# Optimization experiments

Hardware: AMD Instinct MI355X
Metric: run time of the kernel (lower is better)

The kernel has to match this reference:

```python
import jax, jax.numpy as jnp
import numpy as np

SIG_DEPTH = 4  # matches sig_depth init arg


def _outer(a, b):
    # flattened tensor product: [B, m] x [B, n] -> [B, m*n] (row-major, matches signatory layout)
    return (a[:, :, None] * b[:, None, :]).reshape(a.shape[0], -1)


def setup_inputs() -> dict:
    key = jax.random.key(0)
    k1, k2 = jax.random.split(key)
    B, L, Cin = 64, 256, 7
    out_dim = 512
    C = Cin + 1
    sig_channels = sum(C ** k for k in range(1, SIG_DEPTH + 1))  # 4680
    inp = jax.random.normal(k1, (B, L, Cin), dtype=jnp.float32)
    W = jax.random.normal(k2, (out_dim, sig_channels), dtype=jnp.float32) * 0.02
    b = jnp.zeros((out_dim,), dtype=jnp.float32)
    return {"inp": inp, "W": W, "b": b}


def reference(inp, W, b):
    B, L, Cin = inp.shape
    # Augment: prepend time channel linspace(0, 1, L), keep original channels
    t = jnp.broadcast_to(jnp.linspace(0.0, 1.0, L, dtype=inp.dtype)[None, :, None], (B, L, 1))
    x = jnp.concatenate([t, inp], axis=-1)  # [B, L, C]
    C = Cin + 1
    d = SIG_DEPTH
    dx = jnp.transpose(x[:, 1:] - x[:, :-1], (1, 0, 2))  # [L-1, B, C] increments
    init = tuple(jnp.zeros((B, C ** (k + 1)), x.dtype) for k in range(d))  # identity signature (all zero levels)

    def step(levels, v):
        # exp(v) in the truncated tensor algebra: e_k = v^{(x)k} / k!
        e = [v]
        for k in range(1, d):
            e.append(_outer(e[-1], v) / (k + 1))
        # Chen's identity: new_k = a_k + e_k + sum_{i=1}^{k-1} a_i (x) e_{k-i}
        new = []
        for k in range(d):
            acc = levels[k] + e[k]
            for i in range(k):
                acc = acc + _outer(levels[i], e[k - 1 - i])
            new.append(acc)
        sig = jnp.concatenate(new, axis=-1)  # [B, sig_channels]
        return tuple(new), sig

    _, sigs = jax.lax.scan(step, init, dx)  # [L-1, B, sig_channels] (stream=True)
    sigs = jnp.transpose(sigs, (1, 0, 2))   # [B, L-1, sig_channels]
    return sigs @ W.T + b                   # [B, L-1, out_dim]
```

## Files before the change

kernel.cpp:

```cpp
#include <hip/hip_runtime.h>
#include <hip/hip_bf16.h>

#define BATCH 64
#define LSEQ 256
#define CIN 7
#define CC 8
#define NSIG 4680
#define KPAD 4736
#define TSTEPS 255
#define ODIM 512
#define NCHUNK 16
#define CH 16
#define NKT 74
#define BM 256
#define BN 128
#define WCVT_BLK 592

typedef __attribute__((ext_vector_type(8))) unsigned short ushort8;
typedef __attribute__((ext_vector_type(8))) __bf16 bf16x8;
typedef __attribute__((ext_vector_type(4))) float f32x4;

__device__ __forceinline__ unsigned short f2bf(float x) {
    __hip_bfloat16 h = __float2bfloat16(x);
    return *(unsigned short*)&h;
}

#define GLDS16(gp, lp)                                                      \
    __builtin_amdgcn_global_load_lds(                                       \
        (const __attribute__((address_space(1))) void*)(gp),                \
        (__attribute__((address_space(3))) void*)(lp), 16, 0, 0)

__global__ __launch_bounds__(512) void prep_kernel(const float* __restrict__ inp,
                                                   float* __restrict__ ckpt,
                                                   const float* __restrict__ W,
                                                   unsigned short* __restrict__ Wb,
                                                   int nb) {
    __shared__ float sDx[TSTEPS * CC];
    const int bx  = blockIdx.x;
    const int tid = threadIdx.x;

    if (bx < 4 * nb) {
        const int b = bx >> 2, q = bx & 3;
        const float* ip = inp + (size_t)b * LSEQ * CIN;
        for (int i = tid; i < TSTEPS * CC; i += 512) {
            int t = i >> 3, c = i & 7;
            sDx[i] = (c == 0) ? (1.0f / 255.0f)
                              : ip[(t + 1) * CIN + (c - 1)] - ip[t * CIN + (c - 1)];
        }
        __syncthreads();

        const int o  = q * 128 + (tid >> 2);
        const int e2 = tid & 3;
        const int i1 = o >> 6, i2 = (o >> 3) & 7, i3 = o & 7;
        float a1 = 0.0f, a2 = 0.0f, a3 = 0.0f, a4a = 0.0f, a4b = 0.0f;

        for (int t = 0; t < 240; ++t) {
            const float* v = &sDx[t * CC];
            const float va = v[i1], vb = v[i2], vc = v[i3];
            const float vA = v[e2], vB = v[e2 + 4];
            const float e3s = va * vb * vc * (1.0f / 6.0f);
            const float T4 = e3s * 0.25f + a1 * vb * vc * (1.0f / 6.0f)
                           + a2 * vc * 0.5f + a3;
            a4a += vA * T4;
            a4b += vB * T4;
            a3 += e3s + (a1 * vb * 0.5f + a2) * vc;
            a2 += vb * (0.5f * va + a1);
            a1 += va;

            if (((t + 1) & 15) == 0) {
                const int c = ((t + 1) >> 4) - 1;
                float* cp = ckpt + ((size_t)b * 15 + c) * NSIG;
                cp[584 + o * 8 + e2]     = a4a;
                cp[584 + o * 8 + e2 + 4] = a4b;
                if (e2 == 0) {
                    cp[72 + o] = a3;
                    if ((o & 7) == 0)  cp[8 + (o >> 3)] = a2;
                    if ((o & 63) == 0) cp[i1] = a1;
                }
            }
        }
    } else {
        const int vid = (bx - 4 * nb) * 512 + tid;
        if (vid < ODIM * (KPAD / 8)) {
            const int n = vid / (KPAD / 8);
            const int g = vid - n * (KPAD / 8);
            ushort8 pk;
            if (g < NSIG / 8) {
                const float* wp = W + (size_t)n * NSIG + g * 8;
                float4 f0 = *(const float4*)wp;
                float4 f1 = *(const float4*)(wp + 4);
                pk[0] = f2bf(f0.x); pk[1] = f2bf(f0.y);
                pk[2] = f2bf(f0.z); pk[3] = f2bf(f0.w);
                pk[4] = f2bf(f1.x); pk[5] = f2bf(f1.y);
                pk[6] = f2bf(f1.z); pk[7] = f2bf(f1.w);
            } else {
#pragma unroll
                for (int e = 0; e < 8; ++e) pk[e] = 0;
            }
            *(ushort8*)(Wb + (size_t)n * KPAD + g * 8) = pk;
        }
    }
}

__global__ __launch_bounds__(512) void sig_write_kernel(const float* __restrict__ inp,
                                                        const float* __restrict__ ckpt,
                                                        unsigned short* __restrict__ sig) {
    __shared__ float sDx[CH * CC];

    const int chunk = blockIdx.x;
    const int b     = blockIdx.y;
    const int tid   = threadIdx.x;
    const int t0    = chunk * CH;
    const int t1    = (chunk == NCHUNK - 1) ? TSTEPS : t0 + CH;

    const float* ip = inp + (size_t)b * LSEQ * CIN;
    for (int i = tid; i < (t1 - t0) * CC; i += 512) {
        int t = t0 + (i >> 3), c = i & 7;
        sDx[i] = (c == 0) ? (1.0f / 255.0f)
                          : ip[(t + 1) * CIN + (c - 1)] - ip[t * CIN + (c - 1)];
    }
    __syncthreads();

    const int i1 = tid >> 6;
    const int i2 = (tid >> 3) & 7;
    const int i3 = tid & 7;

    float a1own, a2own, a3;
    float a4[8];
    if (chunk == 0) {
        a1own = a2own = a3 = 0.0f;
#pragma unroll
        for (int e = 0; e < 8; ++e) a4[e] = 0.0f;
    } else {
        const float* cp = ckpt + ((size_t)b * 15 + (chunk - 1)) * NSIG;
        a1own = cp[i1];
        a2own = cp[8 + (tid >> 3)];
        a3    = cp[72 + tid];
        float4 q0 = *(const float4*)&cp[584 + tid * 8];
        float4 q1 = *(const float4*)&cp[584 + tid * 8 + 4];
        a4[0] = q0.x; a4[1] = q0.y; a4[2] = q0.z; a4[3] = q0.w;
        a4[4] = q1.x; a4[5] = q1.y; a4[6] = q1.z; a4[7] = q1.w;
    }

    for (int t = t0; t < t1; ++t) {
        const float* v = &sDx[(t - t0) * CC];
        const float4 vlo = *(const float4*)&v[0];
        const float4 vhi = *(const float4*)&v[4];
        const float va = v[i1], vb = v[i2], vc = v[i3];
        const float e3s = va * vb * vc * (1.0f / 6.0f);
        const float T4 = e3s * 0.25f + a1own * vb * vc * (1.0f / 6.0f)
                       + a2own * vc * 0.5f + a3;
        a4[0] += vlo.x * T4; a4[1] += vlo.y * T4;
        a4[2] += vlo.z * T4; a4[3] += vlo.w * T4;
        a4[4] += vhi.x * T4; a4[5] += vhi.y * T4;
        a4[6] += vhi.z * T4; a4[7] += vhi.w * T4;
        a3 += e3s + (a1own * vb * 0.5f + a2own) * vc;
        a2own += vb * (0.5f * va + a1own);
        a1own += va;

        unsigned short* row = sig + ((size_t)b * TSTEPS + t) * KPAD;
        ushort8 pack;
#pragma unroll
        for (int e = 0; e < 8; ++e) pack[e] = f2bf(a4[e]);
        *(ushort8*)(row + 584 + tid * 8) = pack;
        row[72 + tid] = f2bf(a3);
        if ((tid & 63) == 0) row[i1] = f2bf(a1own);
        if ((tid & 7) == 0) row[8 + (tid >> 3)] = f2bf(a2own);
        if (tid >= 448 && tid < 504) row[4232 + tid] = 0;
    }
}

__global__ __launch_bounds__(512) void gemm_kernel(const unsigned short* __restrict__ A,
                                                   const unsigned short* __restrict__ Wb,
                                                   const float* __restrict__ bias,
                                                   float* __restrict__ out,
                                                   int Mrows) {
    __shared__ unsigned short As[3][BM * 64];
    __shared__ unsigned short Bs[3][BN * 64];

    const int tid = threadIdx.x;
    int nt, mt;
    if (gridDim.y == 64) {
        const int li = blockIdx.y * 4 + blockIdx.x;
        const int x  = li & 7;
        const int j  = li >> 3;
        mt = x * 8 + (j >> 2);
        nt = j & 3;
    } else {
        nt = blockIdx.x; mt = blockIdx.y;
    }
    const int lane = tid & 63;
    const int wv   = tid >> 6;
    const int wr   = wv >> 1;
    const int wc   = wv & 1;
    const int lr   = lane & 15;
    const int lq   = lane >> 4;
    const int sb   = lr & 7;

    const f32x4 z4 = {0.0f, 0.0f, 0.0f, 0.0f};
    f32x4 acc[4][4];
#pragma unroll
    for (int i = 0; i < 4; ++i)
#pragma unroll
        for (int j = 0; j < 4; ++j) acc[i][j] = z4;

    const int srow = tid >> 3;
    const int gcb  = (tid & 7) ^ (srow & 7);
    const int scol = gcb * 8;

    const unsigned short* aptr[4];
    const unsigned short* bptr[2];
#pragma unroll
    for (int i = 0; i < 4; ++i) {
        int gr = mt * BM + i * 64 + srow;
        if (gr >= Mrows) gr = 0;
        aptr[i] = A + (size_t)gr * KPAD + scol;
    }
#pragma unroll
    for (int i = 0; i < 2; ++i)
        bptr[i] = Wb + (size_t)(nt * BN + i * 64 + srow) * KPAD + scol;

    const int kel0 = ((lq)     ^ sb) * 8;
    const int kel1 = ((4 + lq) ^ sb) * 8;
    const int aoff = (wr * 64 + lr) * 64;
    const int boff = (wc * 64 + lr) * 64;

#define STAGE_ALL(buf, koff)                                                \
    do {                                                                    \
        _Pragma("unroll")                                                   \
        for (int i_ = 0; i_ < 4; ++i_)                                      \
            GLDS16(aptr[i_] + (koff),                                       \
                   ((char*)As[buf]) + i_ * 8192 + tid * 16);                \
        _Pragma("unroll")                                                   \
        for (int i_ = 0; i_ < 2; ++i_)                                      \
            GLDS16(bptr[i_] + (koff),                                       \
                   ((char*)Bs[buf]) + i_ * 8192 + tid * 16);                \
    } while (0)

    STAGE_ALL(0, 0);
    STAGE_ALL(1, 64);
    asm volatile("s_waitcnt vmcnt(6)" ::: "memory");
    __builtin_amdgcn_sched_barrier(0);
    __builtin_amdgcn_s_barrier();
    __builtin_amdgcn_sched_barrier(0);

    bf16x8 afP[4], bfP[4], afN[4], bfN[4];
    {
        const unsigned short* as0 = &As[0][0];
        const unsigned short* bs0 = &Bs[0][0];
#pragma unroll
        for (int i = 0; i < 4; ++i)
            afP[i] = *(const bf16x8*)&as0[aoff + i * 1024 + kel0];
#pragma unroll
        for (int j = 0; j < 4; ++j)
            bfP[j] = *(const bf16x8*)&bs0[boff + j * 1024 + kel0];
    }
    __builtin_amdgcn_sched_barrier(0);

    int cur = 0, nxt = 1, nn = 2;
    for (int t = 0; t < NKT; ++t) {
        const unsigned short* as = &As[0][0] + cur * (BM * 64);
        const unsigned short* bs = &Bs[0][0] + cur * (BN * 64);

#pragma unroll
        for (int i = 0; i < 4; ++i)
            afN[i] = *(const bf16x8*)&as[aoff + i * 1024 + kel1];
#pragma unroll
        for (int j = 0; j < 4; ++j)
            bfN[j] = *(const bf16x8*)&bs[boff + j * 1024 + kel1];
        if (t + 2 < NKT) STAGE_ALL(nn, (t + 2) * 64);
        __builtin_amdgcn_sched_barrier(0);

        asm volatile("s_waitcnt lgkmcnt(8)" ::: "memory");
        __builtin_amdgcn_sched_barrier(0);
        __builtin_amdgcn_s_setprio(1);
#pragma unroll
        for (int i = 0; i < 4; ++i)
#pragma unroll
            for (int j = 0; j < 4; ++j)
                acc[i][j] = __builtin_amdgcn_mfma_f32_16x16x32_bf16(
                    afP[i], bfP[j], acc[i][j], 0, 0, 0);
        __builtin_amdgcn_s_setprio(0);
        __builtin_amdgcn_sched_barrier(0);

        asm volatile("s_waitcnt lgkmcnt(0)" ::: "memory");
        __builtin_amdgcn_sched_barrier(0);
        if (t + 1 < NKT) {
            if (t + 2 < NKT) {
                asm volatile("s_waitcnt vmcnt(6)" ::: "memory");
            } else {
                asm volatile("s_waitcnt vmcnt(0)" ::: "memory");
            }
            __builtin_amdgcn_sched_barrier(0);
            __builtin_amdgcn_s_barrier();
            __builtin_amdgcn_sched_barrier(0);
            const unsigned short* asn = &As[0][0] + nxt * (BM * 64);
            const unsigned short* bsn = &Bs[0][0] + nxt * (BN * 64);
#pragma unroll
            for (int i = 0; i < 4; ++i)
                afP[i] = *(const bf16x8*)&asn[aoff + i * 1024 + kel0];
#pragma unroll
            for (int j = 0; j < 4; ++j)
                bfP[j] = *(const bf16x8*)&bsn[boff + j * 1024 + kel0];
            __builtin_amdgcn_sched_barrier(0);
        }

        __builtin_amdgcn_s_setprio(1);
#pragma unroll
        for (int i = 0; i < 4; ++i)
#pragma unroll
            for (int j = 0; j < 4; ++j)
                acc[i][j] = __builtin_amdgcn_mfma_f32_16x16x32_bf16(
                    afN[i], bfN[j], acc[i][j], 0, 0, 0);
        __builtin_amdgcn_s_setprio(0);
        __builtin_amdgcn_sched_barrier(0);

        const int tmp = cur; cur = nxt; nxt = nn; nn = tmp;
    }

    float bn[4];
#pragma unroll
    for (int j = 0; j < 4; ++j)
        bn[j] = bias[nt * BN + wc * 64 + j * 16 + lr];

#pragma unroll
    for (int i = 0; i < 4; ++i) {
        const int mbase = mt * BM + wr * 64 + i * 16 + lq * 4;
#pragma unroll
        for (int r = 0; r < 4; ++r) {
            const int m = mbase + r;
            if (m < Mrows) {
#pragma unroll
                for (int j = 0; j < 4; ++j) {
                    const int n = nt * BN + wc * 64 + j * 16 + lr;
                    out[(size_t)m * ODIM + n] = acc[i][j][r] + bn[j];
                }
            }
        }
    }
#undef STAGE_ALL
}

extern "C" void kernel_launch(void* const* d_in, const int* in_sizes, int n_in,
                              void* d_out, int out_size, void* d_ws, size_t ws_size,
                              hipStream_t stream) {
    const float* inp  = (const float*)d_in[0];
    const float* W    = (const float*)d_in[1];
    const float* bias = (const float*)d_in[2];
    float* out = (float*)d_out;

    const size_t wbBytes = (size_t)ODIM * KPAD * sizeof(unsigned short);
    const size_t sigPB   = (size_t)TSTEPS * KPAD * sizeof(unsigned short);
    const size_t ckptPB  = (size_t)15 * NSIG * sizeof(float);
    const size_t perB    = sigPB + ckptPB;

    int nbMax = (int)((ws_size - wbBytes) / perB);
    if (nbMax > BATCH) nbMax = BATCH;
    if (nbMax < 1) nbMax = 1;

    unsigned short* sig  = (unsigned short*)d_ws;
    float*          ckpt = (float*)((char*)d_ws + (size_t)nbMax * sigPB);
    unsigned short* Wb   = (unsigned short*)((char*)d_ws + (ws_size - wbBytes));

    for (int b0 = 0; b0 < BATCH; b0 += nbMax) {
        const int nb = (b0 + nbMax <= BATCH) ? nbMax : (BATCH - b0);
        const int Mrows = nb * TSTEPS;
        const float* ipb = inp + (size_t)b0 * LSEQ * CIN;
        prep_kernel<<<4 * nb + WCVT_BLK, 512, 0, stream>>>(ipb, ckpt, W, Wb, nb);
        sig_write_kernel<<<dim3(NCHUNK, nb), 512, 0, stream>>>(ipb, ckpt, sig);
        gemm_kernel<<<dim3(ODIM / BN, (Mrows + BM - 1) / BM), 512, 0, stream>>>(
            sig, Wb, bias, out + (size_t)b0 * TSTEPS * ODIM, Mrows);
    }
}
```

Before: 146.2 us.

## Fuse prep, signature write and GEMM into one cooperative kernel with grid syncs

Replaces the three-kernel sequence with a single cooperative launch of 256 blocks. Grid-wide syncs separate three phases: checkpoint computation, W conversion plus signature writing, and the bf16 MFMA GEMM. The goal is to remove launch gaps and inter-kernel drains. The cost is fixed parallelism per phase: the W conversion and signature chunks now loop over 256 blocks instead of using wider grids. The path only runs when the workspace can hold the full batch.

```diff
diff --git a/kernel.cpp b/kernel.cpp
--- a/kernel.cpp
+++ b/kernel.cpp
@@ -1,5 +1,8 @@
 #include <hip/hip_runtime.h>
 #include <hip/hip_bf16.h>
+#include <hip/hip_cooperative_groups.h>
+
+namespace cg = cooperative_groups;
 
 #define BATCH 64
 #define LSEQ 256
@@ -14,6 +17,7 @@
 #define NKT 74
 #define BM 256
 #define BN 128
+#define M_TOTAL 16320
 #define WCVT_BLK 592
 
 typedef __attribute__((ext_vector_type(8))) unsigned short ushort8;
@@ -29,6 +33,317 @@
     __builtin_amdgcn_global_load_lds(                                       \
         (const __attribute__((address_space(1))) void*)(gp),                \
         (__attribute__((address_space(3))) void*)(lp), 16, 0, 0)
+
+__global__ __launch_bounds__(512) void fused_kernel(const float* __restrict__ inp,
+                                                    const float* __restrict__ W,
+                                                    const float* __restrict__ bias,
+                                                    float* __restrict__ out,
+                                                    unsigned short* __restrict__ sig,
+                                                    float* __restrict__ ckpt,
+                                                    unsigned short* __restrict__ Wb) {
+    __shared__ __align__(16) char ldsraw[147456];
+    const int bx  = blockIdx.x;
+    const int tid = threadIdx.x;
+    cg::grid_group grid = cg::this_grid();
+
+    {
+        float* sDx = (float*)ldsraw;
+        const int b = bx >> 2, q = bx & 3;
+        const float* ip = inp + (size_t)b * LSEQ * CIN;
+        for (int i = tid; i < TSTEPS * CC; i += 512) {
+            int t = i >> 3, c = i & 7;
+            sDx[i] = (c == 0) ? (1.0f / 255.0f)
+                              : ip[(t + 1) * CIN + (c - 1)] - ip[t * CIN + (c - 1)];
+        }
+        __syncthreads();
+
+        const int o  = q * 128 + (tid >> 2);
+        const int e2 = tid & 3;
+        const int i1 = o >> 6, i2 = (o >> 3) & 7, i3 = o & 7;
+        float a1 = 0.0f, a2 = 0.0f, a3 = 0.0f, a4a = 0.0f, a4b = 0.0f;
+
+        for (int t = 0; t < 240; ++t) {
+            const float* v = &sDx[t * CC];
+            const float va = v[i1], vb = v[i2], vc = v[i3];
+            const float vA = v[e2], vB = v[e2 + 4];
+            const float e3s = va * vb * vc * (1.0f / 6.0f);
+            const float T4 = e3s * 0.25f + a1 * vb * vc * (1.0f / 6.0f)
+                           + a2 * vc * 0.5f + a3;
+            a4a += vA * T4;
+            a4b += vB * T4;
+            a3 += e3s + (a1 * vb * 0.5f + a2) * vc;
+            a2 += vb * (0.5f * va + a1);
+            a1 += va;
+
+            if (((t + 1) & 15) == 0) {
+                const int c = ((t + 1) >> 4) - 1;
+                float* cp = ckpt + ((size_t)b * 15 + c) * NSIG;
+                cp[584 + o * 8 + e2]     = a4a;
+                cp[584 + o * 8 + e2 + 4] = a4b;
+                if (e2 == 0) {
+                    cp[72 + o] = a3;
+                    if ((o & 7) == 0)  cp[8 + (o >> 3)] = a2;
+                    if ((o & 63) == 0) cp[i1] = a1;
+                }
+            }
+        }
+    }
+    grid.sync();
+
+    {
+        for (int u = bx; u < WCVT_BLK; u += 256) {
+            const int vid = u * 512 + tid;
+            if (vid < ODIM * (KPAD / 8)) {
+                const int n = vid / (KPAD / 8);
+                const int g = vid - n * (KPAD / 8);
+                ushort8 pk;
+                if (g < NSIG / 8) {
+                    const float* wp = W + (size_t)n * NSIG + g * 8;
+                    float4 f0 = *(const float4*)wp;
+                    float4 f1 = *(const float4*)(wp + 4);
+                    pk[0] = f2bf(f0.x); pk[1] = f2bf(f0.y);
+                    pk[2] = f2bf(f0.z); pk[3] = f2bf(f0.w);
+                    pk[4] = f2bf(f1.x); pk[5] = f2bf(f1.y);
+                    pk[6] = f2bf(f1.z); pk[7] = f2bf(f1.w);
+                } else {
+#pragma unroll
+                    for (int e = 0; e < 8; ++e) pk[e] = 0;
+                }
+                *(ushort8*)(Wb + (size_t)n * KPAD + g * 8) = pk;
+            }
+        }
+
+        float* sDx = (float*)ldsraw;
+        for (int u = bx; u < NCHUNK * BATCH; u += 256) {
+            const int chunk = u & 15;
+            const int b     = u >> 4;
+            const int t0    = chunk * CH;
+            const int t1    = (chunk == NCHUNK - 1) ? TSTEPS : t0 + CH;
+
+            __syncthreads();
+            const float* ip = inp + (size_t)b * LSEQ * CIN;
+            for (int i = tid; i < (t1 - t0) * CC; i += 512) {
+                int t = t0 + (i >> 3), c = i & 7;
+                sDx[i] = (c == 0) ? (1.0f / 255.0f)
+                                  : ip[(t + 1) * CIN + (c - 1)] - ip[t * CIN + (c - 1)];
+            }
+            __syncthreads();
+
+            const int i1 = tid >> 6;
+            const int i2 = (tid >> 3) & 7;
+            const int i3 = tid & 7;
+
+            float a1own, a2own, a3;
+            float a4[8];
+            if (chunk == 0) {
+                a1own = a2own = a3 = 0.0f;
+#pragma unroll
+                for (int e = 0; e < 8; ++e) a4[e] = 0.0f;
+            } else {
+                const float* cp = ckpt + ((size_t)b * 15 + (chunk - 1)) * NSIG;
+                a1own = cp[i1];
+                a2own = cp[8 + (tid >> 3)];
+                a3    = cp[72 + tid];
+                float4 q0 = *(const float4*)&cp[584 + tid * 8];
+                float4 q1 = *(const float4*)&cp[584 + tid * 8 + 4];
+                a4[0] = q0.x; a4[1] = q0.y; a4[2] = q0.z; a4[3] = q0.w;
+                a4[4] = q1.x; a4[5] = q1.y; a4[6] = q1.z; a4[7] = q1.w;
+            }
+
+            for (int t = t0; t < t1; ++t) {
+                const float* v = &sDx[(t - t0) * CC];
+                const float4 vlo = *(const float4*)&v[0];
+                const float4 vhi = *(const float4*)&v[4];
+                const float va = v[i1], vb = v[i2], vc = v[i3];
+                const float e3s = va * vb * vc * (1.0f / 6.0f);
+                const float T4 = e3s * 0.25f + a1own * vb * vc * (1.0f / 6.0f)
+                               + a2own * vc * 0.5f + a3;
+                a4[0] += vlo.x * T4; a4[1] += vlo.y * T4;
+                a4[2] += vlo.z * T4; a4[3] += vlo.w * T4;
+                a4[4] += vhi.x * T4; a4[5] += vhi.y * T4;
+                a4[6] += vhi.z * T4; a4[7] += vhi.w * T4;
+                a3 += e3s + (a1own * vb * 0.5f + a2own) * vc;
+                a2own += vb * (0.5f * va + a1own);
+                a1own += va;
+
+                unsigned short* row = sig + ((size_t)b * TSTEPS + t) * KPAD;
+                ushort8 pack;
+#pragma unroll
+                for (int e = 0; e < 8; ++e) pack[e] = f2bf(a4[e]);
+                *(ushort8*)(row + 584 + tid * 8) = pack;
+                row[72 + tid] = f2bf(a3);
+                if ((tid & 63) == 0) row[i1] = f2bf(a1own);
+                if ((tid & 7) == 0) row[8 + (tid >> 3)] = f2bf(a2own);
+                if (tid >= 448 && tid < 504) row[4232 + tid] = 0;
+            }
+        }
+    }
+    grid.sync();
+
+    {
+        unsigned short (*As)[BM * 64] = (unsigned short (*)[BM * 64])(ldsraw);
+        unsigned short (*Bs)[BN * 64] =
+            (unsigned short (*)[BN * 64])(ldsraw + 3 * BM * 64 * 2);
+
+        const int li = bx;
+        const int x  = li & 7;
+        const int j  = li >> 3;
+        const int mt = x * 8 + (j >> 2);
+        const int nt = j & 3;
+        const int Mrows = M_TOTAL;
+
+        const int lane = tid & 63;
+        const int wv   = tid >> 6;
+        const int wr   = wv >> 1;
+        const int wc   = wv & 1;
+        const int lr   = lane & 15;
+        const int lq   = lane >> 4;
+        const int sb   = lr & 7;
+
+        const f32x4 z4 = {0.0f, 0.0f, 0.0f, 0.0f};
+        f32x4 acc[4][4];
+#pragma unroll
+        for (int i = 0; i < 4; ++i)
+#pragma unroll
+            for (int j2 = 0; j2 < 4; ++j2) acc[i][j2] = z4;
+
+        const int srow = tid >> 3;
+        const int gcb  = (tid & 7) ^ (srow & 7);
+        const int scol = gcb * 8;
+
+        const unsigned short* aptr[4];
+        const unsigned short* bptr[2];
+#pragma unroll
+        for (int i = 0; i < 4; ++i) {
+            int gr = mt * BM + i * 64 + srow;
+            if (gr >= Mrows) gr = 0;
+            aptr[i] = sig + (size_t)gr * KPAD + scol;
+        }
+#pragma unroll
+        for (int i = 0; i < 2; ++i)
+            bptr[i] = Wb + (size_t)(nt * BN + i * 64 + srow) * KPAD + scol;
+
+        const int kel0 = ((lq)     ^ sb) * 8;
+        const int kel1 = ((4 + lq) ^ sb) * 8;
+        const int aoff = (wr * 64 + lr) * 64;
+        const int boff = (wc * 64 + lr) * 64;
+
+#define STAGE_ALL(buf, koff)                                                \
+    do {                                                                    \
+        _Pragma("unroll")                                                   \
+        for (int i_ = 0; i_ < 4; ++i_)                                      \
+            GLDS16(aptr[i_] + (koff),                                       \
+                   ((char*)As[buf]) + i_ * 8192 + tid * 16);                \
+        _Pragma("unroll")                                                   \
+        for (int i_ = 0; i_ < 2; ++i_)                                      \
+            GLDS16(bptr[i_] + (koff),                                       \
+                   ((char*)Bs[buf]) + i_ * 8192 + tid * 16);                \
+    } while (0)
+
+        STAGE_ALL(0, 0);
+        STAGE_ALL(1, 64);
+        asm volatile("s_waitcnt vmcnt(6)" ::: "memory");
+        __builtin_amdgcn_sched_barrier(0);
+        __builtin_amdgcn_s_barrier();
+        __builtin_amdgcn_sched_barrier(0);
+
+        bf16x8 afP[4], bfP[4], afN[4], bfN[4];
+        {
+            const unsigned short* as0 = &As[0][0];
+            const unsigned short* bs0 = &Bs[0][0];
+#pragma unroll
+            for (int i = 0; i < 4; ++i)
+                afP[i] = *(const bf16x8*)&as0[aoff + i * 1024 + kel0];
+#pragma unroll
+            for (int j2 = 0; j2 < 4; ++j2)
+                bfP[j2] = *(const bf16x8*)&bs0[boff + j2 * 1024 + kel0];
+        }
+        __builtin_amdgcn_sched_barrier(0);
+
+        int cur = 0, nxt = 1, nn = 2;
+        for (int t = 0; t < NKT; ++t) {
+            const unsigned short* as = &As[0][0] + cur * (BM * 64);
+            const unsigned short* bs = &Bs[0][0] + cur * (BN * 64);
+
+#pragma unroll
+            for (int i = 0; i < 4; ++i)
+                afN[i] = *(const bf16x8*)&as[aoff + i * 1024 + kel1];
+#pragma unroll
+            for (int j2 = 0; j2 < 4; ++j2)
+                bfN[j2] = *(const bf16x8*)&bs[boff + j2 * 1024 + kel1];
+            if (t + 2 < NKT) STAGE_ALL(nn, (t + 2) * 64);
+            __builtin_amdgcn_sched_barrier(0);
+
+            asm volatile("s_waitcnt lgkmcnt(8)" ::: "memory");
+            __builtin_amdgcn_sched_barrier(0);
+            __builtin_amdgcn_s_setprio(1);
+#pragma unroll
+            for (int i = 0; i < 4; ++i)
+#pragma unroll
+                for (int j2 = 0; j2 < 4; ++j2)
+                    acc[i][j2] = __builtin_amdgcn_mfma_f32_16x16x32_bf16(
+                        afP[i], bfP[j2], acc[i][j2], 0, 0, 0);
+            __builtin_amdgcn_s_setprio(0);
+            __builtin_amdgcn_sched_barrier(0);
+
+            asm volatile("s_waitcnt lgkmcnt(0)" ::: "memory");
+            __builtin_amdgcn_sched_barrier(0);
+            if (t + 1 < NKT) {
+                if (t + 2 < NKT) {
+                    asm volatile("s_waitcnt vmcnt(6)" ::: "memory");
+                } else {
+                    asm volatile("s_waitcnt vmcnt(0)" ::: "memory");
+                }
+                __builtin_amdgcn_sched_barrier(0);
+                __builtin_amdgcn_s_barrier();
+                __builtin_amdgcn_sched_barrier(0);
+                const unsigned short* asn = &As[0][0] + nxt * (BM * 64);
+                const unsigned short* bsn = &Bs[0][0] + nxt * (BN * 64);
+#pragma unroll
+                for (int i = 0; i < 4; ++i)
+                    afP[i] = *(const bf16x8*)&asn[aoff + i * 1024 + kel0];
+#pragma unroll
+                for (int j2 = 0; j2 < 4; ++j2)
+                    bfP[j2] = *(const bf16x8*)&bsn[boff + j2 * 1024 + kel0];
+                __builtin_amdgcn_sched_barrier(0);
+            }
+
+            __builtin_amdgcn_s_setprio(1);
+#pragma unroll
+            for (int i = 0; i < 4; ++i)
+#pragma unroll
+                for (int j2 = 0; j2 < 4; ++j2)
+                    acc[i][j2] = __builtin_amdgcn_mfma_f32_16x16x32_bf16(
+                        afN[i], bfN[j2], acc[i][j2], 0, 0, 0);
+            __builtin_amdgcn_s_setprio(0);
+            __builtin_amdgcn_sched_barrier(0);
+
+            const int tmp = cur; cur = nxt; nxt = nn; nn = tmp;
+        }
+
+        float bn[4];
+#pragma unroll
+        for (int j2 = 0; j2 < 4; ++j2)
+            bn[j2] = bias[nt * BN + wc * 64 + j2 * 16 + lr];
+
+#pragma unroll
+        for (int i = 0; i < 4; ++i) {
+            const int mbase = mt * BM + wr * 64 + i * 16 + lq * 4;
+#pragma unroll
+            for (int r = 0; r < 4; ++r) {
+                const int m = mbase + r;
+                if (m < Mrows) {
+#pragma unroll
+                    for (int j2 = 0; j2 < 4; ++j2) {
+                        const int n = nt * BN + wc * 64 + j2 * 16 + lr;
+                        out[(size_t)m * ODIM + n] = acc[i][j2][r] + bn[j2];
+                    }
+                }
+            }
+        }
+#undef STAGE_ALL
+    }
+}
 
 __global__ __launch_bounds__(512) void prep_kernel(const float* __restrict__ inp,
                                                    float* __restrict__ ckpt,
@@ -362,13 +677,26 @@
     float*          ckpt = (float*)((char*)d_ws + (size_t)nbMax * sigPB);
     unsigned short* Wb   = (unsigned short*)((char*)d_ws + (ws_size - wbBytes));
 
-    for (int b0 = 0; b0 < BATCH; b0 += nbMax) {
-        const int nb = (b0 + nbMax <= BATCH) ? nbMax : (BATCH - b0);
-        const int Mrows = nb * TSTEPS;
-        const float* ipb = inp + (size_t)b0 * LSEQ * CIN;
-        prep_kernel<<<4 * nb + WCVT_BLK, 512, 0, stream>>>(ipb, ckpt, W, Wb, nb);
-        sig_write_kernel<<<dim3(NCHUNK, nb), 512, 0, stream>>>(ipb, ckpt, sig);
-        gemm_kernel<<<dim3(ODIM / BN, (Mrows + BM - 1) / BM), 512, 0, stream>>>(
-            sig, Wb, bias, out + (size_t)b0 * TSTEPS * ODIM, Mrows);
+    if (nbMax >= BATCH) {
+        const float* a0 = inp;
+        const float* a1 = W;
+        const float* a2 = bias;
+        float* a3 = out;
+        unsigned short* a4 = sig;
+        float* a5 = ckpt;
+        unsigned short* a6 = Wb;
+        void* kargs[7] = {&a0, &a1, &a2, &a3, &a4, &a5, &a6};
+        hipLaunchCooperativeKernel((void*)fused_kernel, dim3(256), dim3(512),
+                                   kargs, 0, stream);
+    } else {
+        for (int b0 = 0; b0 < BATCH; b0 += nbMax) {
+            const int nb = (b0 + nbMax <= BATCH) ? nbMax : (BATCH - b0);
+            const int Mrows = nb * TSTEPS;
+            const float* ipb = inp + (size_t)b0 * LSEQ * CIN;
+            prep_kernel<<<4 * nb + WCVT_BLK, 512, 0, stream>>>(ipb, ckpt, W, Wb, nb);
+            sig_write_kernel<<<dim3(NCHUNK, nb), 512, 0, stream>>>(ipb, ckpt, sig);
+            gemm_kernel<<<dim3(ODIM / BN, (Mrows + BM - 1) / BM), 512, 0, stream>>>(
+                sig, Wb, bias, out + (size_t)b0 * TSTEPS * ODIM, Mrows);
+        }
     }
 }
```

New measurement: 208.4 us. 1.43x slower.
